# Optimization experiments

Measured on AMD Instinct MI355X. Metric: run time of the kernel, lower is better.

Reference implementation:

```python
import jax, jax.numpy as jnp
import numpy as np

N_NODES = 50000


def _gcn_conv(x, W, b, src, dst, norm, n_nodes):
    # x: [N, Fin], W: [Fin, Fout]
    h = x @ W                                   # [N, Fout]
    msg = h[src] * norm[:, None]                # [E+N, Fout] edge messages
    out = jax.ops.segment_sum(msg, dst, num_segments=n_nodes)
    return out + b


def reference(x, edge_index, W1, b1, W2, b2):
    n = x.shape[0]
    # add self-loops (PyG GCNConv default add_self_loops=True)
    loop = jnp.arange(n, dtype=edge_index.dtype)
    src = jnp.concatenate([edge_index[0], loop])
    dst = jnp.concatenate([edge_index[1], loop])
    # symmetric degree normalization: deg over destination with unit weights
    deg = jax.ops.segment_sum(jnp.ones_like(dst, dtype=x.dtype), dst, num_segments=n)
    dinv = jnp.where(deg > 0, jax.lax.rsqrt(deg), 0.0)
    norm = dinv[src] * dinv[dst]                # [E+N]
    h = _gcn_conv(x, W1, b1, src, dst, norm, n)
    h = jax.nn.relu(h)
    out = _gcn_conv(h, W2, b2, src, dst, norm, n)
    return out


def setup_inputs() -> dict:
    key = jax.random.key(0)
    k1, k2, k3, k4 = jax.random.split(key, 4)
    n, e, fin, hid, fout = N_NODES, 800000, 128, 128, 64
    x = jax.random.normal(k1, (n, fin), dtype=jnp.float32)
    edge_index = jax.random.randint(k2, (2, e), 0, n, dtype=jnp.int64)
    # Glorot-ish init for linear weights, zero bias (PyG default)
    W1 = jax.random.normal(k3, (fin, hid), dtype=jnp.float32) / np.sqrt(fin)
    b1 = jnp.zeros((hid,), dtype=jnp.float32)
    W2 = jax.random.normal(k4, (hid, fout), dtype=jnp.float32) / np.sqrt(hid)
    b2 = jnp.zeros((fout,), dtype=jnp.float32)
    return {"x": x, "edge_index": edge_index, "W1": W1, "b1": b1, "W2": W2, "b2": b2}
```

## Files before the change

### kernel.cpp

```cpp
#include <hip/hip_runtime.h>
#include <hip/hip_bf16.h>


constexpr int FIN = 128;
constexpr int HID = 128;
constexpr int FOUT = 64;
constexpr int CAP = 48;
constexpr int NPB = 98;
constexpr int BCAP = 3072;
constexpr int OVF_MAX = 65536;

typedef __attribute__((ext_vector_type(8))) short s16x8;
typedef __attribute__((ext_vector_type(4))) float f32x4;

static __device__ __forceinline__ float bf2f(__hip_bfloat16 v) { return __bfloat162float(v); }
static __device__ __forceinline__ float lo2f(unsigned u) { union { unsigned i; float f; } c; c.i = u << 16; return c.f; }
static __device__ __forceinline__ float hi2f(unsigned u) { union { unsigned i; float f; } c; c.i = u & 0xffff0000u; return c.f; }
static __device__ __forceinline__ unsigned short f2bfu(float f) {
    __hip_bfloat16 h = __float2bfloat16(f);
    union { __hip_bfloat16 h; unsigned short u; } c; c.h = h; return c.u;
}
static __device__ __forceinline__ unsigned pack2(float a, float b) {
    return (unsigned)f2bfu(a) | ((unsigned)f2bfu(b) << 16);
}
static __device__ __forceinline__ void acc_add(float* acc, uint4 v) {
    acc[0] += lo2f(v.x); acc[1] += hi2f(v.x);
    acc[2] += lo2f(v.y); acc[3] += hi2f(v.y);
    acc[4] += lo2f(v.z); acc[5] += hi2f(v.z);
    acc[6] += lo2f(v.w); acc[7] += hi2f(v.w);
}

__global__ __launch_bounds__(256) void k_detect(const unsigned* __restrict__ xw,
                                                const int* __restrict__ eiw,
                                                int E, int* __restrict__ flags,
                                                int* __restrict__ gcur,
                                                int* __restrict__ cnt, int N) {
    for (long i = (long)blockIdx.x * 256 + threadIdx.x; i < N; i += (long)gridDim.x * 256)
        cnt[i] = 0;
    if (blockIdx.x != 0) return;
    for (int i = threadIdx.x; i < 514; i += 256) gcur[i] = 0;
    __shared__ int s_bf16like, s_oddnz;
    if (threadIdx.x == 0) { s_bf16like = 0; s_oddnz = 0; }
    __syncthreads();
    int c = 0;
    for (int i = threadIdx.x; i < 4096; i += 256) {
        unsigned ex = ((xw[i] & 0xffffu) >> 7) & 0xffu;
        if (ex >= 117u && ex <= 130u) c++;
    }
    atomicAdd(&s_bf16like, c);
    int nz = 0;
    for (int i = threadIdx.x; i < 2048; i += 256)
        if (eiw[2 * i + 1] != 0) nz++;
    atomicAdd(&s_oddnz, nz);
    __syncthreads();
    if (threadIdx.x == 0) {
        flags[0] = (s_bf16like < 2048) ? 1 : 0;
        flags[1] = (s_oddnz == 0) ? 1 : 0;
    }
}

__global__ __launch_bounds__(256) void k_binA(const int* __restrict__ ei, int E, int N,
                                              int nbuk,
                                              int* __restrict__ gcur,
                                              unsigned* __restrict__ pairs,
                                              int2* __restrict__ ovfA,
                                              int* __restrict__ ovfAcnt,
                                              const int* __restrict__ flags) {
    __shared__ int hist[512];
    __shared__ int gbase[512];
    const int tid = threadIdx.x;
    const long base = (long)blockIdx.x * 2048;
    const bool i64 = flags[1] != 0;
    int se[8], de[8];
    for (int b = tid; b < nbuk; b += 256) hist[b] = 0;
    __syncthreads();
#pragma unroll
    for (int j = 0; j < 8; ++j) {
        long i = base + j * 256 + tid;
        int s = 0, d = -1;
        if (i < E) {
            if (i64) { s = ((const int2*)ei)[i].x; d = ((const int2*)(ei + 2 * (long)E))[i].x; }
            else     { s = ei[i]; d = ei[(long)E + i]; }
            if ((unsigned)s >= (unsigned)N || (unsigned)d >= (unsigned)N) d = -1;
        }
        se[j] = s; de[j] = d;
        if (d >= 0) atomicAdd(&hist[d / NPB], 1);
    }
    __syncthreads();
    for (int b = tid; b < nbuk; b += 256) {
        int h = hist[b];
        gbase[b] = h > 0 ? atomicAdd(&gcur[b], h) : 0;
        hist[b] = 0;
    }
    __syncthreads();
#pragma unroll
    for (int j = 0; j < 8; ++j) {
        int d = de[j];
        if (d < 0) continue;
        int b = d / NPB;
        int p = gbase[b] + atomicAdd(&hist[b], 1);
        if (p < BCAP) {
            pairs[(long)b * BCAP + p] = ((unsigned)(d - b * NPB) << 16) | (unsigned)se[j];
        } else {
            int op = atomicAdd(ovfAcnt, 1);
            if (op < OVF_MAX) ovfA[op] = make_int2(d, se[j]);
        }
    }
}

__global__ __launch_bounds__(256) void k_binB(const int* __restrict__ gcur,
                                              const unsigned* __restrict__ pairs,
                                              const int2* __restrict__ ovfA,
                                              const int* __restrict__ ovfAcnt,
                                              int* __restrict__ cnt,
                                              unsigned short* __restrict__ slots,
                                              int2* __restrict__ ovf2,
                                              int* __restrict__ ovf2cnt, int N) {
    __shared__ int cntL[NPB];
    __shared__ __align__(16) unsigned short slotsL[NPB * CAP];
    const int b = blockIdx.x;
    const int tid = threadIdx.x;
    const int d0 = b * NPB;
    const int nd = min(NPB, N - d0);
    if (nd <= 0) return;
    for (int i = tid; i < NPB; i += 256) cntL[i] = 0;
    __syncthreads();
    const int c = min(gcur[b], BCAP);
    const unsigned* pb = pairs + (long)b * BCAP;
    for (int i = tid; i < c; i += 256) {
        unsigned p = pb[i];
        int ld = p >> 16;
        int pos = atomicAdd(&cntL[ld], 1);
        if (pos < CAP) {
            slotsL[ld * CAP + pos] = (unsigned short)(p & 0xffffu);
        } else {
            int op = atomicAdd(ovf2cnt, 1);
            if (op < OVF_MAX) ovf2[op] = make_int2(d0 + ld, (int)(p & 0xffffu));
        }
    }
    int na = *ovfAcnt; na = na < OVF_MAX ? na : OVF_MAX;
    for (int i = tid; i < na; i += 256) {
        int2 p = ovfA[i];
        int ld = p.x - d0;
        if ((unsigned)ld < (unsigned)nd) {
            int pos = atomicAdd(&cntL[ld], 1);
            if (pos < CAP) {
                slotsL[ld * CAP + pos] = (unsigned short)p.y;
            } else {
                int op = atomicAdd(ovf2cnt, 1);
                if (op < OVF_MAX) ovf2[op] = p;
            }
        }
    }
    __syncthreads();
    for (int i = tid; i < nd; i += 256) cnt[d0 + i] = cntL[i];
    const uint4* sv = (const uint4*)slotsL;
    uint4* gv = (uint4*)(slots + (long)d0 * CAP);
    const int total8 = (nd * CAP) >> 3;
    for (int i = tid; i < total8; i += 256) gv[i] = sv[i];
}

__global__ __launch_bounds__(256) void k_build_direct(const int* __restrict__ ei, int E, int N,
                                                      int* __restrict__ cnt,
                                                      int* __restrict__ slots,
                                                      int2* __restrict__ ovf2,
                                                      int* __restrict__ ovf2cnt,
                                                      const int* __restrict__ flags) {
    long i = (long)blockIdx.x * 256 + threadIdx.x;
    if (i >= E) return;
    int s, d;
    if (flags[1]) { s = ((const int2*)ei)[i].x; d = ((const int2*)(ei + 2 * (long)E))[i].x; }
    else          { s = ei[i]; d = ei[(long)E + i]; }
    if ((unsigned)s >= (unsigned)N || (unsigned)d >= (unsigned)N) return;
    int pos = atomicAdd(&cnt[d], 1);
    if (pos < CAP) {
        slots[(long)d * CAP + pos] = s;
    } else {
        int op = atomicAdd(ovf2cnt, 1);
        if (op < OVF_MAX) ovf2[op] = make_int2(d, s);
    }
}

template<int CT, int SPLIT>
__global__ __launch_bounds__(256) void k_gemm(const void* __restrict__ Xp, int x_follows_flag,
                                              const void* __restrict__ Wp,
                                              const int* __restrict__ cnt,
                                              __hip_bfloat16* __restrict__ G,
                                              const int* __restrict__ flags, int N) {
    constexpr int C = CT * 16;
    __shared__ __align__(16) short Wt[C * 136];
    const bool f32m = flags[0] != 0;
    const bool xf32 = (x_follows_flag != 0) && f32m;
    const int tid = threadIdx.x;
    for (int i = tid; i < 128 * C; i += 256) {
        int k = i / C, n = i % C;
        float wv = f32m ? ((const float*)Wp)[(long)k * C + n]
                        : bf2f(((const __hip_bfloat16*)Wp)[(long)k * C + n]);
        Wt[n * 136 + k] = (short)f2bfu(wv);
    }
    __syncthreads();
    const int w = tid >> 6, lane = tid & 63;
    const int m = lane & 15, quad = lane >> 4;
    const int rowA = blockIdx.x * 64 + w * 16 + m;
    const int rowc = rowA < N ? rowA : N - 1;
    s16x8 afr[4];
#pragma unroll
    for (int kc = 0; kc < 4; ++kc) {
        const int k0 = kc * 32 + quad * 8;
        if (!xf32) {
            afr[kc] = *(const s16x8*)((const __hip_bfloat16*)Xp + (long)rowc * 128 + k0);
        } else {
            const float* p = (const float*)Xp + (long)rowc * 128 + k0;
            s16x8 t;
#pragma unroll
            for (int j = 0; j < 8; ++j) t[j] = (short)f2bfu(p[j]);
            afr[kc] = t;
        }
    }
    const int rbase = blockIdx.x * 64 + w * 16 + quad * 4;
    float dv[4];
#pragma unroll
    for (int r = 0; r < 4; ++r) {
        int rr = min(rbase + r, N - 1);
        dv[r] = rsqrtf((float)(cnt[rr] + 1));
    }
#pragma unroll
    for (int ct = 0; ct < CT; ++ct) {
        f32x4 acc = {0.f, 0.f, 0.f, 0.f};
#pragma unroll
        for (int kc = 0; kc < 4; ++kc) {
            s16x8 bfr = *(const s16x8*)&Wt[(ct * 16 + m) * 136 + kc * 32 + quad * 8];
            acc = __builtin_amdgcn_mfma_f32_16x16x32_bf16(afr[kc], bfr, acc, 0, 0, 0);
        }
#pragma unroll
        for (int r = 0; r < 4; ++r) {
            int rr = rbase + r;
            if (rr < N) {
                long off;
                if (SPLIT) {
                    const int plane = ct / (CT / 2);
                    const int cp = (ct % (CT / 2)) * 16 + m;
                    off = (long)plane * N * (C / 2) + (long)rr * (C / 2) + cp;
                } else {
                    off = (long)rr * C + ct * 16 + m;
                }
                G[off] = __float2bfloat16(dv[r] * acc[r]);
            }
        }
    }
}

__global__ __launch_bounds__(256) void k_gather_half(const __hip_bfloat16* __restrict__ Gp,
                                                     const int* __restrict__ cnt,
                                                     const unsigned short* __restrict__ slots,
                                                     const int2* __restrict__ ovf2,
                                                     const int* __restrict__ ovf2cnt,
                                                     const void* __restrict__ b1,
                                                     __hip_bfloat16* __restrict__ h1,
                                                     const int* __restrict__ flags,
                                                     int N, int P) {
    const int tid = threadIdx.x;
    const int grp = tid >> 3, lane = tid & 7;
    const int node = blockIdx.x * 32 + grp;
    if (node >= N) return;
    const int cd = cnt[node];
    const float wself = rsqrtf((float)(cd + 1));
    const int m = cd < CAP ? cd : CAP;
    const unsigned short* sl = slots + (long)node * CAP;
    float acc[8] = {0, 0, 0, 0, 0, 0, 0, 0};
    acc_add(acc, ((const uint4*)(Gp + (long)node * 64))[lane]);
    int i = 0;
    for (; i + 7 < m; i += 8) {
        int s0 = sl[i], s1 = sl[i + 1], s2 = sl[i + 2], s3 = sl[i + 3];
        int s4 = sl[i + 4], s5 = sl[i + 5], s6 = sl[i + 6], s7 = sl[i + 7];
        uint4 v0 = ((const uint4*)(Gp + (long)s0 * 64))[lane];
        uint4 v1 = ((const uint4*)(Gp + (long)s1 * 64))[lane];
        uint4 v2 = ((const uint4*)(Gp + (long)s2 * 64))[lane];
        uint4 v3 = ((const uint4*)(Gp + (long)s3 * 64))[lane];
        uint4 v4 = ((const uint4*)(Gp + (long)s4 * 64))[lane];
        uint4 v5 = ((const uint4*)(Gp + (long)s5 * 64))[lane];
        uint4 v6 = ((const uint4*)(Gp + (long)s6 * 64))[lane];
        uint4 v7 = ((const uint4*)(Gp + (long)s7 * 64))[lane];
        acc_add(acc, v0); acc_add(acc, v1); acc_add(acc, v2); acc_add(acc, v3);
        acc_add(acc, v4); acc_add(acc, v5); acc_add(acc, v6); acc_add(acc, v7);
    }
    for (; i + 3 < m; i += 4) {
        int s0 = sl[i], s1 = sl[i + 1], s2 = sl[i + 2], s3 = sl[i + 3];
        uint4 v0 = ((const uint4*)(Gp + (long)s0 * 64))[lane];
        uint4 v1 = ((const uint4*)(Gp + (long)s1 * 64))[lane];
        uint4 v2 = ((const uint4*)(Gp + (long)s2 * 64))[lane];
        uint4 v3 = ((const uint4*)(Gp + (long)s3 * 64))[lane];
        acc_add(acc, v0); acc_add(acc, v1); acc_add(acc, v2); acc_add(acc, v3);
    }
    for (; i < m; ++i)
        acc_add(acc, ((const uint4*)(Gp + (long)sl[i] * 64))[lane]);
    if (cd > CAP) {
        int oc = *ovf2cnt; oc = oc < OVF_MAX ? oc : OVF_MAX;
        for (int j = 0; j < oc; ++j)
            if (ovf2[j].x == node)
                acc_add(acc, ((const uint4*)(Gp + (long)ovf2[j].y * 64))[lane]);
    }
    const bool f32m = flags[0] != 0;
    const int c0 = P * 64 + lane * 8;
    float bv[8];
    if (f32m) {
        const float4* bp = (const float4*)((const float*)b1 + c0);
        float4 b0 = bp[0], b1v = bp[1];
        bv[0] = b0.x; bv[1] = b0.y; bv[2] = b0.z; bv[3] = b0.w;
        bv[4] = b1v.x; bv[5] = b1v.y; bv[6] = b1v.z; bv[7] = b1v.w;
    } else {
        uint4 b = *(const uint4*)((const __hip_bfloat16*)b1 + c0);
        bv[0] = lo2f(b.x); bv[1] = hi2f(b.x); bv[2] = lo2f(b.y); bv[3] = hi2f(b.y);
        bv[4] = lo2f(b.z); bv[5] = hi2f(b.z); bv[6] = lo2f(b.w); bv[7] = hi2f(b.w);
    }
    float o[8];
#pragma unroll
    for (int c = 0; c < 8; ++c) {
        float v = wself * acc[c] + bv[c];
        o[c] = v > 0.f ? v : 0.f;
    }
    uint4 pv = { pack2(o[0], o[1]), pack2(o[2], o[3]), pack2(o[4], o[5]), pack2(o[6], o[7]) };
    ((uint4*)(h1 + (long)node * 128 + P * 64))[lane] = pv;
}

template<int F, int LAYER1, typename ST>
__global__ __launch_bounds__(256) void k_gather(const __hip_bfloat16* __restrict__ G,
                                                const int* __restrict__ cnt,
                                                const ST* __restrict__ slots,
                                                const int2* __restrict__ ovf2,
                                                const int* __restrict__ ovf2cnt,
                                                const void* __restrict__ bias,
                                                void* __restrict__ outp,
                                                const int* __restrict__ flags, int N) {
    constexpr int L = F / 8;
    constexpr int NODES = 256 / L;
    const int tid = threadIdx.x;
    const int grp = tid / L, lane = tid % L;
    const int node = blockIdx.x * NODES + grp;
    if (node >= N) return;
    const int cd = cnt[node];
    const float wself = rsqrtf((float)(cd + 1));
    const int m = cd < CAP ? cd : CAP;
    const ST* sl = slots + (long)node * CAP;
    float acc[8] = {0, 0, 0, 0, 0, 0, 0, 0};
    acc_add(acc, ((const uint4*)(G + (long)node * F))[lane]);
    int i = 0;
    for (; i + 7 < m; i += 8) {
        int s0 = sl[i], s1 = sl[i + 1], s2 = sl[i + 2], s3 = sl[i + 3];
        int s4 = sl[i + 4], s5 = sl[i + 5], s6 = sl[i + 6], s7 = sl[i + 7];
        uint4 v0 = ((const uint4*)(G + (long)s0 * F))[lane];
        uint4 v1 = ((const uint4*)(G + (long)s1 * F))[lane];
        uint4 v2 = ((const uint4*)(G + (long)s2 * F))[lane];
        uint4 v3 = ((const uint4*)(G + (long)s3 * F))[lane];
        uint4 v4 = ((const uint4*)(G + (long)s4 * F))[lane];
        uint4 v5 = ((const uint4*)(G + (long)s5 * F))[lane];
        uint4 v6 = ((const uint4*)(G + (long)s6 * F))[lane];
        uint4 v7 = ((const uint4*)(G + (long)s7 * F))[lane];
        acc_add(acc, v0); acc_add(acc, v1); acc_add(acc, v2); acc_add(acc, v3);
        acc_add(acc, v4); acc_add(acc, v5); acc_add(acc, v6); acc_add(acc, v7);
    }
    for (; i + 3 < m; i += 4) {
        int s0 = sl[i], s1 = sl[i + 1], s2 = sl[i + 2], s3 = sl[i + 3];
        uint4 v0 = ((const uint4*)(G + (long)s0 * F))[lane];
        uint4 v1 = ((const uint4*)(G + (long)s1 * F))[lane];
        uint4 v2 = ((const uint4*)(G + (long)s2 * F))[lane];
        uint4 v3 = ((const uint4*)(G + (long)s3 * F))[lane];
        acc_add(acc, v0); acc_add(acc, v1); acc_add(acc, v2); acc_add(acc, v3);
    }
    for (; i < m; ++i)
        acc_add(acc, ((const uint4*)(G + (long)sl[i] * F))[lane]);
    if (cd > CAP) {
        int oc = *ovf2cnt; oc = oc < OVF_MAX ? oc : OVF_MAX;
        for (int j = 0; j < oc; ++j)
            if (ovf2[j].x == node)
                acc_add(acc, ((const uint4*)(G + (long)ovf2[j].y * F))[lane]);
    }
    const bool f32m = flags[0] != 0;
    const int c0 = lane * 8;
    float bv[8];
    if (f32m) {
        const float4* bp = (const float4*)((const float*)bias + c0);
        float4 b0 = bp[0], b1 = bp[1];
        bv[0] = b0.x; bv[1] = b0.y; bv[2] = b0.z; bv[3] = b0.w;
        bv[4] = b1.x; bv[5] = b1.y; bv[6] = b1.z; bv[7] = b1.w;
    } else {
        uint4 b = *(const uint4*)((const __hip_bfloat16*)bias + c0);
        bv[0] = lo2f(b.x); bv[1] = hi2f(b.x); bv[2] = lo2f(b.y); bv[3] = hi2f(b.y);
        bv[4] = lo2f(b.z); bv[5] = hi2f(b.z); bv[6] = lo2f(b.w); bv[7] = hi2f(b.w);
    }
    float o[8];
#pragma unroll
    for (int c = 0; c < 8; ++c) {
        float v = wself * acc[c] + bv[c];
        o[c] = (LAYER1 && v < 0.f) ? 0.f : v;
    }
    if (LAYER1 || !f32m) {
        uint4 pv = { pack2(o[0], o[1]), pack2(o[2], o[3]), pack2(o[4], o[5]), pack2(o[6], o[7]) };
        ((uint4*)outp)[(long)node * L + lane] = pv;
    } else {
        float4* op = (float4*)((float*)outp + (long)node * F + c0);
        op[0] = make_float4(o[0], o[1], o[2], o[3]);
        op[1] = make_float4(o[4], o[5], o[6], o[7]);
    }
}

extern "C" void kernel_launch(void* const* d_in, const int* in_sizes, int n_in,
                              void* d_out, int out_size, void* d_ws, size_t ws_size,
                              hipStream_t stream) {
    const void* x  = d_in[0];
    const int*  ei = (const int*)d_in[1];
    const void* W1 = d_in[2];
    const void* b1 = d_in[3];
    const void* W2 = d_in[4];
    const void* b2 = d_in[5];

    const int N = in_sizes[0] / FIN;
    const int E = in_sizes[1] / 2;
    const int nbuk = (N + NPB - 1) / NPB;

    char* ws = (char*)d_ws;
    int*   flags   = (int*)ws;
    int*   gcur    = (int*)(ws + 4096);
    int*   ovfAcnt = gcur + 512;
    int*   ovf2cnt = gcur + 513;
    int*   cnt     = (int*)(ws + 65536);
    int2*  ovfA    = (int2*)(ws + 524288);
    int2*  ovf2    = (int2*)(ws + 1048576);
    unsigned short* slots16 = (unsigned short*)(ws + 2097152);
    int*   slots32 = (int*)(ws + 2097152);
    __hip_bfloat16* g  = (__hip_bfloat16*)(ws + 11730944);
    __hip_bfloat16* g2 = g;
    unsigned* pairs = (unsigned*)(ws + 24530944);
    __hip_bfloat16* h1 = (__hip_bfloat16*)(ws + 24530944);

    const int GB = (N + 63) / 64;
    const int AB = (E + 2047) / 2048;
    const int EB = (E + 255) / 256;

    k_detect<<<64, 256, 0, stream>>>((const unsigned*)x, ei, E, flags, gcur, cnt, N);

    if (N <= 65536 && nbuk <= 512) {
        k_binA<<<AB, 256, 0, stream>>>(ei, E, N, nbuk, gcur, pairs, ovfA, ovfAcnt, flags);
        k_binB<<<nbuk, 256, 0, stream>>>(gcur, pairs, ovfA, ovfAcnt, cnt, slots16, ovf2, ovf2cnt, N);
        k_gemm<8, 1><<<GB, 256, 0, stream>>>(x, 1, W1, cnt, g, flags, N);
        k_gather_half<<<(N + 31) / 32, 256, 0, stream>>>(g, cnt, slots16, ovf2, ovf2cnt, b1, h1, flags, N, 0);
        k_gather_half<<<(N + 31) / 32, 256, 0, stream>>>(g + (long)N * 64, cnt, slots16, ovf2, ovf2cnt, b1, h1, flags, N, 1);
        k_gemm<4, 0><<<GB, 256, 0, stream>>>(h1, 0, W2, cnt, g2, flags, N);
        k_gather<64, 0, unsigned short><<<(N + 31) / 32, 256, 0, stream>>>(
            g2, cnt, slots16, ovf2, ovf2cnt, b2, d_out, flags, N);
    } else {
        k_build_direct<<<EB, 256, 0, stream>>>(ei, E, N, cnt, slots32, ovf2, ovf2cnt, flags);
        k_gemm<8, 0><<<GB, 256, 0, stream>>>(x, 1, W1, cnt, g, flags, N);
        k_gather<128, 1, int><<<(N + 15) / 16, 256, 0, stream>>>(
            g, cnt, slots32, ovf2, ovf2cnt, b1, h1, flags, N);
        k_gemm<4, 0><<<GB, 256, 0, stream>>>(h1, 0, W2, cnt, g2, flags, N);
        k_gather<64, 0, int><<<(N + 31) / 32, 256, 0, stream>>>(
            g2, cnt, slots32, ovf2, ovf2cnt, b2, d_out, flags, N);
    }
}
```

Measured before the change: 202.7 us.

## Fuse first GEMM with edge binning into one kernel, move degree scaling to gather

Merges the layer-1 feature GEMM and the first edge-binning pass into a single launch whose blocks pick their role by block index, so the compute-bound GEMM and the memory-bound binning can run at the same time. Because the GEMM now runs before degrees are known, source-degree normalization moves into the gather, which reads a per-node dinv array that binB computes. The node-count zeroing in the detect kernel is skipped on this path and detect runs as a single block. In exchange, the gather does an extra scattered dinv load per edge, and the fused kernel needs about 34 KB of dynamic shared memory, which may limit occupancy for the binning blocks.

Result: faster. 193.0 us (-4.8%).

```diff
diff --git a/kernel.cpp b/kernel.cpp
--- a/kernel.cpp
+++ b/kernel.cpp
@@ -29,14 +29,21 @@
     acc[4] += lo2f(v.z); acc[5] += hi2f(v.z);
     acc[6] += lo2f(v.w); acc[7] += hi2f(v.w);
 }
+static __device__ __forceinline__ void acc_fma(float* acc, uint4 v, float w) {
+    acc[0] += w * lo2f(v.x); acc[1] += w * hi2f(v.x);
+    acc[2] += w * lo2f(v.y); acc[3] += w * hi2f(v.y);
+    acc[4] += w * lo2f(v.z); acc[5] += w * hi2f(v.z);
+    acc[6] += w * lo2f(v.w); acc[7] += w * hi2f(v.w);
+}
 
 __global__ __launch_bounds__(256) void k_detect(const unsigned* __restrict__ xw,
                                                 const int* __restrict__ eiw,
                                                 int E, int* __restrict__ flags,
                                                 int* __restrict__ gcur,
-                                                int* __restrict__ cnt, int N) {
-    for (long i = (long)blockIdx.x * 256 + threadIdx.x; i < N; i += (long)gridDim.x * 256)
-        cnt[i] = 0;
+                                                int* __restrict__ cnt, int N, int zero_cnt) {
+    if (zero_cnt)
+        for (long i = (long)blockIdx.x * 256 + threadIdx.x; i < N; i += (long)gridDim.x * 256)
+            cnt[i] = 0;
     if (blockIdx.x != 0) return;
     for (int i = threadIdx.x; i < 514; i += 256) gcur[i] = 0;
     __shared__ int s_bf16like, s_oddnz;
@@ -59,51 +66,103 @@
     }
 }
 
-__global__ __launch_bounds__(256) void k_binA(const int* __restrict__ ei, int E, int N,
-                                              int nbuk,
+__global__ __launch_bounds__(256) void k_mega(const void* __restrict__ Xp,
+                                              const void* __restrict__ Wp,
+                                              const int* __restrict__ ei, int E, int N,
+                                              int nbuk, int GB,
                                               int* __restrict__ gcur,
                                               unsigned* __restrict__ pairs,
                                               int2* __restrict__ ovfA,
                                               int* __restrict__ ovfAcnt,
+                                              __hip_bfloat16* __restrict__ G,
                                               const int* __restrict__ flags) {
-    __shared__ int hist[512];
-    __shared__ int gbase[512];
+    extern __shared__ __align__(16) char smem[];
     const int tid = threadIdx.x;
-    const long base = (long)blockIdx.x * 2048;
-    const bool i64 = flags[1] != 0;
-    int se[8], de[8];
-    for (int b = tid; b < nbuk; b += 256) hist[b] = 0;
-    __syncthreads();
-#pragma unroll
-    for (int j = 0; j < 8; ++j) {
-        long i = base + j * 256 + tid;
-        int s = 0, d = -1;
-        if (i < E) {
-            if (i64) { s = ((const int2*)ei)[i].x; d = ((const int2*)(ei + 2 * (long)E))[i].x; }
-            else     { s = ei[i]; d = ei[(long)E + i]; }
-            if ((unsigned)s >= (unsigned)N || (unsigned)d >= (unsigned)N) d = -1;
-        }
-        se[j] = s; de[j] = d;
-        if (d >= 0) atomicAdd(&hist[d / NPB], 1);
-    }
-    __syncthreads();
-    for (int b = tid; b < nbuk; b += 256) {
-        int h = hist[b];
-        gbase[b] = h > 0 ? atomicAdd(&gcur[b], h) : 0;
-        hist[b] = 0;
-    }
-    __syncthreads();
-#pragma unroll
-    for (int j = 0; j < 8; ++j) {
-        int d = de[j];
-        if (d < 0) continue;
-        int b = d / NPB;
-        int p = gbase[b] + atomicAdd(&hist[b], 1);
-        if (p < BCAP) {
-            pairs[(long)b * BCAP + p] = ((unsigned)(d - b * NPB) << 16) | (unsigned)se[j];
-        } else {
-            int op = atomicAdd(ovfAcnt, 1);
-            if (op < OVF_MAX) ovfA[op] = make_int2(d, se[j]);
+    if ((int)blockIdx.x < GB) {
+        short* Wt = (short*)smem;
+        const bool f32m = flags[0] != 0;
+        for (int i = tid; i < 128 * 128; i += 256) {
+            int k = i >> 7, n = i & 127;
+            float wv = f32m ? ((const float*)Wp)[(long)k * 128 + n]
+                            : bf2f(((const __hip_bfloat16*)Wp)[(long)k * 128 + n]);
+            Wt[n * 136 + k] = (short)f2bfu(wv);
+        }
+        __syncthreads();
+        const int w = tid >> 6, lane = tid & 63;
+        const int m = lane & 15, quad = lane >> 4;
+        const int rowA = blockIdx.x * 64 + w * 16 + m;
+        const int rowc = rowA < N ? rowA : N - 1;
+        s16x8 afr[4];
+#pragma unroll
+        for (int kc = 0; kc < 4; ++kc) {
+            const int k0 = kc * 32 + quad * 8;
+            if (!f32m) {
+                afr[kc] = *(const s16x8*)((const __hip_bfloat16*)Xp + (long)rowc * 128 + k0);
+            } else {
+                const float* p = (const float*)Xp + (long)rowc * 128 + k0;
+                s16x8 t;
+#pragma unroll
+                for (int j = 0; j < 8; ++j) t[j] = (short)f2bfu(p[j]);
+                afr[kc] = t;
+            }
+        }
+        const int rbase = blockIdx.x * 64 + w * 16 + quad * 4;
+#pragma unroll
+        for (int ct = 0; ct < 8; ++ct) {
+            f32x4 acc = {0.f, 0.f, 0.f, 0.f};
+#pragma unroll
+            for (int kc = 0; kc < 4; ++kc) {
+                s16x8 bfr = *(const s16x8*)&Wt[(ct * 16 + m) * 136 + kc * 32 + quad * 8];
+                acc = __builtin_amdgcn_mfma_f32_16x16x32_bf16(afr[kc], bfr, acc, 0, 0, 0);
+            }
+            const int plane = ct >> 2;
+            const int cp = (ct & 3) * 16 + m;
+#pragma unroll
+            for (int r = 0; r < 4; ++r) {
+                int rr = rbase + r;
+                if (rr < N)
+                    G[(long)plane * N * 64 + (long)rr * 64 + cp] = __float2bfloat16(acc[r]);
+            }
+        }
+    } else {
+        int* hist = (int*)smem;
+        int* gbase = hist + 512;
+        const long base = (long)(blockIdx.x - GB) * 2048;
+        const bool i64 = flags[1] != 0;
+        int se[8], de[8];
+        for (int b = tid; b < nbuk; b += 256) hist[b] = 0;
+        __syncthreads();
+#pragma unroll
+        for (int j = 0; j < 8; ++j) {
+            long i = base + j * 256 + tid;
+            int s = 0, d = -1;
+            if (i < E) {
+                if (i64) { s = ((const int2*)ei)[i].x; d = ((const int2*)(ei + 2 * (long)E))[i].x; }
+                else     { s = ei[i]; d = ei[(long)E + i]; }
+                if ((unsigned)s >= (unsigned)N || (unsigned)d >= (unsigned)N) d = -1;
+            }
+            se[j] = s; de[j] = d;
+            if (d >= 0) atomicAdd(&hist[d / NPB], 1);
+        }
+        __syncthreads();
+        for (int b = tid; b < nbuk; b += 256) {
+            int h = hist[b];
+            gbase[b] = h > 0 ? atomicAdd(&gcur[b], h) : 0;
+            hist[b] = 0;
+        }
+        __syncthreads();
+#pragma unroll
+        for (int j = 0; j < 8; ++j) {
+            int d = de[j];
+            if (d < 0) continue;
+            int b = d / NPB;
+            int p = gbase[b] + atomicAdd(&hist[b], 1);
+            if (p < BCAP) {
+                pairs[(long)b * BCAP + p] = ((unsigned)(d - b * NPB) << 16) | (unsigned)se[j];
+            } else {
+                int op = atomicAdd(ovfAcnt, 1);
+                if (op < OVF_MAX) ovfA[op] = make_int2(d, se[j]);
+            }
         }
     }
 }
@@ -113,6 +172,7 @@
                                               const int2* __restrict__ ovfA,
                                               const int* __restrict__ ovfAcnt,
                                               int* __restrict__ cnt,
+                                              float* __restrict__ dinv,
                                               unsigned short* __restrict__ slots,
                                               int2* __restrict__ ovf2,
                                               int* __restrict__ ovf2cnt, int N) {
@@ -153,7 +213,10 @@
         }
     }
     __syncthreads();
-    for (int i = tid; i < nd; i += 256) cnt[d0 + i] = cntL[i];
+    for (int i = tid; i < nd; i += 256) {
+        cnt[d0 + i] = cntL[i];
+        dinv[d0 + i] = rsqrtf((float)(cntL[i] + 1));
+    }
     const uint4* sv = (const uint4*)slotsL;
     uint4* gv = (uint4*)(slots + (long)d0 * CAP);
     const int total8 = (nd * CAP) >> 3;
@@ -252,6 +315,7 @@
 
 __global__ __launch_bounds__(256) void k_gather_half(const __hip_bfloat16* __restrict__ Gp,
                                                      const int* __restrict__ cnt,
+                                                     const float* __restrict__ dinv,
                                                      const unsigned short* __restrict__ slots,
                                                      const int2* __restrict__ ovf2,
                                                      const int* __restrict__ ovf2cnt,
@@ -264,15 +328,17 @@
     const int node = blockIdx.x * 32 + grp;
     if (node >= N) return;
     const int cd = cnt[node];
-    const float wself = rsqrtf((float)(cd + 1));
+    const float wself = dinv[node];
     const int m = cd < CAP ? cd : CAP;
     const unsigned short* sl = slots + (long)node * CAP;
     float acc[8] = {0, 0, 0, 0, 0, 0, 0, 0};
-    acc_add(acc, ((const uint4*)(Gp + (long)node * 64))[lane]);
+    acc_fma(acc, ((const uint4*)(Gp + (long)node * 64))[lane], wself);
     int i = 0;
     for (; i + 7 < m; i += 8) {
         int s0 = sl[i], s1 = sl[i + 1], s2 = sl[i + 2], s3 = sl[i + 3];
         int s4 = sl[i + 4], s5 = sl[i + 5], s6 = sl[i + 6], s7 = sl[i + 7];
+        float w0 = dinv[s0], w1 = dinv[s1], w2 = dinv[s2], w3 = dinv[s3];
+        float w4 = dinv[s4], w5 = dinv[s5], w6 = dinv[s6], w7 = dinv[s7];
         uint4 v0 = ((const uint4*)(Gp + (long)s0 * 64))[lane];
         uint4 v1 = ((const uint4*)(Gp + (long)s1 * 64))[lane];
         uint4 v2 = ((const uint4*)(Gp + (long)s2 * 64))[lane];
@@ -281,24 +347,29 @@
         uint4 v5 = ((const uint4*)(Gp + (long)s5 * 64))[lane];
         uint4 v6 = ((const uint4*)(Gp + (long)s6 * 64))[lane];
         uint4 v7 = ((const uint4*)(Gp + (long)s7 * 64))[lane];
-        acc_add(acc, v0); acc_add(acc, v1); acc_add(acc, v2); acc_add(acc, v3);
-        acc_add(acc, v4); acc_add(acc, v5); acc_add(acc, v6); acc_add(acc, v7);
+        acc_fma(acc, v0, w0); acc_fma(acc, v1, w1); acc_fma(acc, v2, w2); acc_fma(acc, v3, w3);
+        acc_fma(acc, v4, w4); acc_fma(acc, v5, w5); acc_fma(acc, v6, w6); acc_fma(acc, v7, w7);
     }
     for (; i + 3 < m; i += 4) {
         int s0 = sl[i], s1 = sl[i + 1], s2 = sl[i + 2], s3 = sl[i + 3];
+        float w0 = dinv[s0], w1 = dinv[s1], w2 = dinv[s2], w3 = dinv[s3];
         uint4 v0 = ((const uint4*)(Gp + (long)s0 * 64))[lane];
         uint4 v1 = ((const uint4*)(Gp + (long)s1 * 64))[lane];
         uint4 v2 = ((const uint4*)(Gp + (long)s2 * 64))[lane];
         uint4 v3 = ((const uint4*)(Gp + (long)s3 * 64))[lane];
-        acc_add(acc, v0); acc_add(acc, v1); acc_add(acc, v2); acc_add(acc, v3);
-    }
-    for (; i < m; ++i)
-        acc_add(acc, ((const uint4*)(Gp + (long)sl[i] * 64))[lane]);
+        acc_fma(acc, v0, w0); acc_fma(acc, v1, w1); acc_fma(acc, v2, w2); acc_fma(acc, v3, w3);
+    }
+    for (; i < m; ++i) {
+        int s0 = sl[i];
+        acc_fma(acc, ((const uint4*)(Gp + (long)s0 * 64))[lane], dinv[s0]);
+    }
     if (cd > CAP) {
         int oc = *ovf2cnt; oc = oc < OVF_MAX ? oc : OVF_MAX;
         for (int j = 0; j < oc; ++j)
-            if (ovf2[j].x == node)
-                acc_add(acc, ((const uint4*)(Gp + (long)ovf2[j].y * 64))[lane]);
+            if (ovf2[j].x == node) {
+                int s0 = ovf2[j].y;
+                acc_fma(acc, ((const uint4*)(Gp + (long)s0 * 64))[lane], dinv[s0]);
+            }
     }
     const bool f32m = flags[0] != 0;
     const int c0 = P * 64 + lane * 8;
@@ -424,6 +495,7 @@
     int*   ovfAcnt = gcur + 512;
     int*   ovf2cnt = gcur + 513;
     int*   cnt     = (int*)(ws + 65536);
+    float* dinv    = (float*)(ws + 266240);
     int2*  ovfA    = (int2*)(ws + 524288);
     int2*  ovf2    = (int2*)(ws + 1048576);
     unsigned short* slots16 = (unsigned short*)(ws + 2097152);
@@ -437,18 +509,18 @@
     const int AB = (E + 2047) / 2048;
     const int EB = (E + 255) / 256;
 
-    k_detect<<<64, 256, 0, stream>>>((const unsigned*)x, ei, E, flags, gcur, cnt, N);
-
     if (N <= 65536 && nbuk <= 512) {
-        k_binA<<<AB, 256, 0, stream>>>(ei, E, N, nbuk, gcur, pairs, ovfA, ovfAcnt, flags);
-        k_binB<<<nbuk, 256, 0, stream>>>(gcur, pairs, ovfA, ovfAcnt, cnt, slots16, ovf2, ovf2cnt, N);
-        k_gemm<8, 1><<<GB, 256, 0, stream>>>(x, 1, W1, cnt, g, flags, N);
-        k_gather_half<<<(N + 31) / 32, 256, 0, stream>>>(g, cnt, slots16, ovf2, ovf2cnt, b1, h1, flags, N, 0);
-        k_gather_half<<<(N + 31) / 32, 256, 0, stream>>>(g + (long)N * 64, cnt, slots16, ovf2, ovf2cnt, b1, h1, flags, N, 1);
+        k_detect<<<1, 256, 0, stream>>>((const unsigned*)x, ei, E, flags, gcur, cnt, N, 0);
+        k_mega<<<GB + AB, 256, 34816, stream>>>(x, W1, ei, E, N, nbuk, GB,
+                                                gcur, pairs, ovfA, ovfAcnt, g, flags);
+        k_binB<<<nbuk, 256, 0, stream>>>(gcur, pairs, ovfA, ovfAcnt, cnt, dinv, slots16, ovf2, ovf2cnt, N);
+        k_gather_half<<<(N + 31) / 32, 256, 0, stream>>>(g, cnt, dinv, slots16, ovf2, ovf2cnt, b1, h1, flags, N, 0);
+        k_gather_half<<<(N + 31) / 32, 256, 0, stream>>>(g + (long)N * 64, cnt, dinv, slots16, ovf2, ovf2cnt, b1, h1, flags, N, 1);
         k_gemm<4, 0><<<GB, 256, 0, stream>>>(h1, 0, W2, cnt, g2, flags, N);
         k_gather<64, 0, unsigned short><<<(N + 31) / 32, 256, 0, stream>>>(
             g2, cnt, slots16, ovf2, ovf2cnt, b2, d_out, flags, N);
     } else {
+        k_detect<<<64, 256, 0, stream>>>((const unsigned*)x, ei, E, flags, gcur, cnt, N, 1);
         k_build_direct<<<EB, 256, 0, stream>>>(ei, E, N, cnt, slots32, ovf2, ovf2cnt, flags);
         k_gemm<8, 0><<<GB, 256, 0, stream>>>(x, 1, W1, cnt, g, flags, N);
         k_gather<128, 1, int><<<(N + 15) / 16, 256, 0, stream>>>(
```
